# Performance work log

Measured on AMD Instinct MI355X. Metric: run time of the kernel, lower is better.

## Reference

```python
import jax, jax.numpy as jnp
import numpy as np

N = 10000
E = 160000
F_IN = 64
HID = 128
HEADS = 8
NC = 3
NEG_SLOPE = 0.2
EPS = 1e-16


def setup_inputs() -> dict:
    key = jax.random.key(0)
    ks = jax.random.split(key, 12)
    p = lambda k, shape: jax.random.normal(k, shape, jnp.float32) * 0.1
    return {
        "x": jax.random.normal(ks[0], (N, F_IN), jnp.float32),
        "edge_index": jax.random.randint(ks[1], (2, E), 0, N),
        # conv1: F_IN -> 8 heads x 128, concat -> 1024
        "W1": p(ks[2], (F_IN, HEADS * HID)),
        "a_src1": p(ks[3], (HEADS, HID)),
        "a_dst1": p(ks[4], (HEADS, HID)),
        "b1": jnp.zeros((HEADS * HID,), jnp.float32),
        # conv2: 1024 -> 8 heads x 64, concat -> 512
        "W2": p(ks[5], (HEADS * HID, HEADS * (HID // 2))),
        "a_src2": p(ks[6], (HEADS, HID // 2)),
        "a_dst2": p(ks[7], (HEADS, HID // 2)),
        "b2": jnp.zeros((HEADS * (HID // 2),), jnp.float32),
        # conv3: 512 -> 1 head x 3, mean (concat=False)
        "W3": p(ks[8], (HEADS * (HID // 2), NC)),
        "a_src3": p(ks[9], (1, NC)),
        "a_dst3": p(ks[10], (1, NC)),
        "b3": jnp.zeros((NC,), jnp.float32),
    }


def gat_conv(x, src, dst, W, a_src, a_dst, b, concat):
    """PyG-style GATConv (eval mode, self-loops already in src/dst)."""
    n = x.shape[0]
    H, C = a_src.shape
    h = (x @ W).reshape(n, H, C)                      # [N, H, C]
    s_src = jnp.sum(h * a_src[None], axis=-1)         # [N, H]
    s_dst = jnp.sum(h * a_dst[None], axis=-1)         # [N, H]
    e = jax.nn.leaky_relu(s_src[src] + s_dst[dst], NEG_SLOPE)  # [E, H]
    # segment softmax over incoming edges per destination node
    m = jax.ops.segment_max(e, dst, num_segments=n)   # [N, H]
    ex = jnp.exp(e - m[dst])
    denom = jax.ops.segment_sum(ex, dst, num_segments=n)
    alpha = ex / (denom[dst] + EPS)                   # [E, H]
    msg = h[src] * alpha[:, :, None]                  # [E, H, C]
    out = jax.ops.segment_sum(msg, dst, num_segments=n)  # [N, H, C]
    out = out.reshape(n, H * C) if concat else out.mean(axis=1)
    return out + b


def reference(x, edge_index, W1, a_src1, a_dst1, b1, W2, a_src2, a_dst2, b2, W3, a_src3, a_dst3, b3):
    n = x.shape[0]
    loop = jnp.arange(n, dtype=edge_index.dtype)
    src = jnp.concatenate([edge_index[0], loop])
    dst = jnp.concatenate([edge_index[1], loop])
    h = gat_conv(x, src, dst, W1, a_src1, a_dst1, b1, True)
    h = jax.nn.elu(h)
    h = gat_conv(h, src, dst, W2, a_src2, a_dst2, b2, True)
    h = jax.nn.elu(h)
    h = gat_conv(h, src, dst, W3, a_src3, a_dst3, b3, False)
    return jax.nn.log_softmax(h, axis=1)
```

## Files before the change

### kernel.cpp

```cpp
#include <hip/hip_runtime.h>
#include <math.h>

#define NEG_SLOPE 0.2f
#define EPS_DEN 1e-16f

typedef __attribute__((ext_vector_type(8))) short bf16x8;
typedef __attribute__((ext_vector_type(4))) float f32x4;

__device__ inline void split2(float a, short& hi, short& lo) {
    unsigned u = __float_as_uint(a);
    unsigned uh = (u + 0x8000u) & 0xFFFF0000u;
    float fh = __uint_as_float(uh);
    hi = (short)(uh >> 16);
    float r = a - fh;
    lo = (short)((__float_as_uint(r) + 0x8000u) >> 16);
}

__device__ inline unsigned short f2bf(float f) {
    unsigned u = __float_as_uint(f);
    return (unsigned short)((u + 0x7FFFu + ((u >> 16) & 1u)) >> 16);
}
__device__ inline float bflo(unsigned u) { return __uint_as_float(u << 16); }
__device__ inline float bfhi(unsigned u) { return __uint_as_float(u & 0xFFFF0000u); }

__global__ __launch_bounds__(256) void k_pre(const int* __restrict__ ei, int E, int Nn,
                                             int* __restrict__ counts,
                                             const float* __restrict__ x, short* __restrict__ A1, int Mp,
                                             const float* __restrict__ W1, short* __restrict__ B1t,
                                             const float* __restrict__ W2, short* __restrict__ B2t) {
    __shared__ float s[32][33];
    int t = threadIdx.x;
    int b = blockIdx.x;
    int ET = E + Nn;
    int etb = (ET + 255) / 256;
    int xb = (Mp * 64 + 255) / 256;
    if (b < etb) {
        int e = b * 256 + t;
        if (e < ET) {
            int d = (e < E) ? ei[E + e] : (e - E);
            atomicAdd(&counts[d], 1);
        }
        return;
    }
    b -= etb;
    if (b < xb) {
        int i = b * 256 + t;
        if (i < Mp * 64) {
            int row = i >> 6, c = i & 63;
            float v = (row < Nn) ? x[(size_t)row * 64 + c] : 0.f;
            short hi, lo;
            split2(v, hi, lo);
            A1[(size_t)row * 128 + c] = hi;
            A1[(size_t)row * 128 + 64 + c] = lo;
        }
        return;
    }
    b -= xb;
    const float* W; short* Bt; int K, N, dup, kb, nb;
    if (b < 64) {
        W = W1; Bt = B1t; K = 64; N = 1024; dup = 1;
        kb = b & 1; nb = b >> 1;
    } else {
        b -= 64;
        W = W2; Bt = B2t; K = 1024; N = 512; dup = 0;
        kb = b & 31; nb = b >> 5;
    }
    int k0 = kb * 32, n0 = nb * 32;
    int tx = t & 31, ty = t >> 5;
    for (int r = ty; r < 32; r += 8) s[r][tx] = W[(size_t)(k0 + r) * N + n0 + tx];
    __syncthreads();
    int ldbt = (1 + dup) * K;
    for (int r = ty; r < 32; r += 8) {
        float v = s[tx][r];
        unsigned u = __float_as_uint(v);
        short hi = (short)((u + 0x7FFFu + ((u >> 16) & 1u)) >> 16);
        size_t base = (size_t)(n0 + r) * ldbt + k0 + tx;
        Bt[base] = hi;
        if (dup) Bt[base + K] = hi;
    }
}

__global__ void k_scan(const int* __restrict__ counts, int Nn, int ET, int* __restrict__ row_off) {
    __shared__ int lds[256];
    int t = threadIdx.x;
    int chunk = (Nn + 255) / 256;
    int b0 = t * chunk, b1 = min(Nn, b0 + chunk);
    int s = 0;
    for (int i = b0; i < b1; i++) s += counts[i];
    lds[t] = s;
    __syncthreads();
    #pragma unroll
    for (int d = 1; d < 256; d <<= 1) {
        int v = (t >= d) ? lds[t - d] : 0;
        __syncthreads();
        lds[t] += v;
        __syncthreads();
    }
    int run = (t == 0) ? 0 : lds[t - 1];
    for (int i = b0; i < b1; i++) { row_off[i] = run; run += counts[i]; }
    if (t == 0) row_off[Nn] = ET;
}

__global__ void k_scatter(const int* __restrict__ ei, int E, int Nn,
                          const int* __restrict__ row_off, int* cursor, int* __restrict__ col) {
    int e = blockIdx.x * blockDim.x + threadIdx.x;
    int ET = E + Nn;
    if (e >= ET) return;
    int d = (e < E) ? ei[E + e] : (e - E);
    int s = (e < E) ? ei[e] : (e - E);
    int pos = atomicAdd(&cursor[d], 1);
    col[row_off[d] + pos] = s;
}

__global__ __launch_bounds__(256) void k_mfma_w(const short* __restrict__ A,
                                                const short* __restrict__ B,
                                                unsigned short* __restrict__ C,
                                                const float* __restrict__ a_src,
                                                const float* __restrict__ a_dst,
                                                float* __restrict__ ssrc,
                                                float* __restrict__ sdst,
                                                int M, int N, int Ktot,
                                                int lda, int ldb) {
    __shared__ short As[64 * 32];
    __shared__ short Bs[128 * 32];
    __shared__ float sred[4][64][2];
    int t = threadIdx.x;
    int lane = t & 63;
    int wid = t >> 6;

    int nbx = N >> 7;
    int nb = gridDim.x;
    int q = nb >> 3, r = nb & 7;
    int xcd = blockIdx.x & 7, pos = blockIdx.x >> 3;
    int L = (xcd < r ? xcd * (q + 1) : r * (q + 1) + (xcd - r) * q) + pos;
    int bn = (L % nbx) * 128;
    int bm = (L / nbx) * 64;

    int wm = (wid & 1) * 32, wn = (wid >> 1) * 64;
    int fr = lane & 15, kq = lane >> 4;

    int srow = t >> 2, sslot = t & 3;
    int sko = ((sslot ^ ((srow >> 1) & 3)) << 3);

    f32x4 acc[2][4] = {};

    for (int k0 = 0; k0 < Ktot; k0 += 32) {
        {
            const short* sa = A + (size_t)(bm + srow) * lda + k0 + sko;
            short* da = As + (size_t)(wid << 6) * 8;
            __builtin_amdgcn_global_load_lds((const __attribute__((address_space(1))) void*)sa,
                                             (__attribute__((address_space(3))) void*)da, 16, 0, 0);
            #pragma unroll
            for (int qq = 0; qq < 2; qq++) {
                int v = qq * 256 + t;
                int rowb = v >> 2, slotb = v & 3;
                int skob = ((slotb ^ ((rowb >> 1) & 3)) << 3);
                const short* sb = B + (size_t)(bn + rowb) * ldb + k0 + skob;
                short* db = Bs + (size_t)(qq * 256 + (wid << 6)) * 8;
                __builtin_amdgcn_global_load_lds((const __attribute__((address_space(1))) void*)sb,
                                                 (__attribute__((address_space(3))) void*)db, 16, 0, 0);
            }
        }
        __syncthreads();
        bf16x8 af[2], bfv[4];
        #pragma unroll
        for (int i = 0; i < 2; i++) {
            int rowa = wm + i * 16 + fr;
            af[i] = *(const bf16x8*)(As + rowa * 32 + ((kq ^ ((rowa >> 1) & 3)) << 3));
        }
        #pragma unroll
        for (int j = 0; j < 4; j++) {
            int rowb = wn + j * 16 + fr;
            bfv[j] = *(const bf16x8*)(Bs + rowb * 32 + ((kq ^ ((rowb >> 1) & 3)) << 3));
        }
        #pragma unroll
        for (int i = 0; i < 2; i++)
            #pragma unroll
            for (int j = 0; j < 4; j++)
                acc[i][j] = __builtin_amdgcn_mfma_f32_16x16x32_bf16(af[i], bfv[j], acc[i][j], 0, 0, 0);
        __syncthreads();
    }
    #pragma unroll
    for (int i = 0; i < 2; i++) {
        int rbase = bm + wm + i * 16 + kq * 4;
        #pragma unroll
        for (int j = 0; j < 4; j++) {
            int colc = bn + wn + j * 16 + fr;
            #pragma unroll
            for (int rg = 0; rg < 4; rg++) {
                int rr = rbase + rg;
                if (rr < M) C[(size_t)rr * N + colc] = f2bf(acc[i][j][rg]);
            }
        }
    }
    float asv[4], adv[4];
    #pragma unroll
    for (int j = 0; j < 4; j++) {
        int colc = bn + wn + j * 16 + fr;
        asv[j] = a_src[colc];
        adv[j] = a_dst[colc];
    }
    float ps[8], pd[8];
    #pragma unroll
    for (int i = 0; i < 2; i++)
        #pragma unroll
        for (int rg = 0; rg < 4; rg++) {
            int k8 = i * 4 + rg;
            ps[k8] = acc[i][0][rg] * asv[0] + acc[i][1][rg] * asv[1]
                   + acc[i][2][rg] * asv[2] + acc[i][3][rg] * asv[3];
            pd[k8] = acc[i][0][rg] * adv[0] + acc[i][1][rg] * adv[1]
                   + acc[i][2][rg] * adv[2] + acc[i][3][rg] * adv[3];
        }
    #pragma unroll
    for (int k8 = 0; k8 < 8; k8++) {
        #pragma unroll
        for (int off = 1; off < 16; off <<= 1) {
            ps[k8] += __shfl_xor(ps[k8], off);
            pd[k8] += __shfl_xor(pd[k8], off);
        }
    }
    if (fr == 0) {
        #pragma unroll
        for (int i = 0; i < 2; i++)
            #pragma unroll
            for (int rg = 0; rg < 4; rg++) {
                int rl = wm + i * 16 + kq * 4 + rg;
                sred[wid][rl][0] = ps[i * 4 + rg];
                sred[wid][rl][1] = pd[i * 4 + rg];
            }
    }
    __syncthreads();
    if (wid < 2 && fr == 0) {
        int hh = bn >> 7;
        #pragma unroll
        for (int i = 0; i < 2; i++)
            #pragma unroll
            for (int rg = 0; rg < 4; rg++) {
                int rl = wm + i * 16 + kq * 4 + rg;
                int rr = bm + rl;
                if (rr < M) {
                    ssrc[rr * 8 + hh] = sred[wid][rl][0] + sred[wid + 2][rl][0];
                    sdst[rr * 8 + hh] = sred[wid][rl][1] + sred[wid + 2][rl][1];
                }
            }
    }
}

__global__ __launch_bounds__(256) void k_mfma64(const short* __restrict__ A,
                                                const short* __restrict__ B,
                                                unsigned short* __restrict__ C,
                                                const float* __restrict__ a_src,
                                                const float* __restrict__ a_dst,
                                                float* __restrict__ ssrc,
                                                float* __restrict__ sdst,
                                                int M, int N, int Ktot,
                                                int lda, int ldb) {
    __shared__ short As[64 * 32];
    __shared__ short Bs[64 * 32];
    __shared__ float sred[4][64][2];
    int t = threadIdx.x;
    int lane = t & 63;
    int wid = t >> 6;

    int nbx = N >> 6;
    int nb = gridDim.x;
    int q = nb >> 3, r = nb & 7;
    int xcd = blockIdx.x & 7, pos = blockIdx.x >> 3;
    int L = (xcd < r ? xcd * (q + 1) : r * (q + 1) + (xcd - r) * q) + pos;
    int bn = (L % nbx) * 64;
    int bm = (L / nbx) * 64;

    int wm = (wid >> 1) * 32, wn = (wid & 1) * 32;
    int fr = lane & 15, kq = lane >> 4;

    int srow = t >> 2, sslot = t & 3;
    int sko = ((sslot ^ ((srow >> 1) & 3)) << 3);

    f32x4 acc[2][2] = {};

    for (int k0 = 0; k0 < Ktot; k0 += 32) {
        {
            const short* sa = A + (size_t)(bm + srow) * lda + k0 + sko;
            const short* sb = B + (size_t)(bn + srow) * ldb + k0 + sko;
            short* da = As + (size_t)(wid << 6) * 8;
            short* db = Bs + (size_t)(wid << 6) * 8;
            __builtin_amdgcn_global_load_lds((const __attribute__((address_space(1))) void*)sa,
                                             (__attribute__((address_space(3))) void*)da, 16, 0, 0);
            __builtin_amdgcn_global_load_lds((const __attribute__((address_space(1))) void*)sb,
                                             (__attribute__((address_space(3))) void*)db, 16, 0, 0);
        }
        __syncthreads();
        bf16x8 af[2], bfv[2];
        #pragma unroll
        for (int i = 0; i < 2; i++) {
            int rowa = wm + i * 16 + fr;
            int rowb = wn + i * 16 + fr;
            af[i]  = *(const bf16x8*)(As + rowa * 32 + ((kq ^ ((rowa >> 1) & 3)) << 3));
            bfv[i] = *(const bf16x8*)(Bs + rowb * 32 + ((kq ^ ((rowb >> 1) & 3)) << 3));
        }
        #pragma unroll
        for (int i = 0; i < 2; i++)
            #pragma unroll
            for (int j = 0; j < 2; j++)
                acc[i][j] = __builtin_amdgcn_mfma_f32_16x16x32_bf16(af[i], bfv[j], acc[i][j], 0, 0, 0);
        __syncthreads();
    }
    #pragma unroll
    for (int i = 0; i < 2; i++) {
        int rbase = bm + wm + i * 16 + kq * 4;
        #pragma unroll
        for (int j = 0; j < 2; j++) {
            int colc = bn + wn + j * 16 + fr;
            #pragma unroll
            for (int rg = 0; rg < 4; rg++) {
                int rr = rbase + rg;
                if (rr < M) C[(size_t)rr * N + colc] = f2bf(acc[i][j][rg]);
            }
        }
    }
    float asv[2], adv[2];
    #pragma unroll
    for (int j = 0; j < 2; j++) {
        int colc = bn + wn + j * 16 + fr;
        asv[j] = a_src[colc];
        adv[j] = a_dst[colc];
    }
    float ps[8], pd[8];
    #pragma unroll
    for (int i = 0; i < 2; i++)
        #pragma unroll
        for (int rg = 0; rg < 4; rg++) {
            int k8 = i * 4 + rg;
            ps[k8] = acc[i][0][rg] * asv[0] + acc[i][1][rg] * asv[1];
            pd[k8] = acc[i][0][rg] * adv[0] + acc[i][1][rg] * adv[1];
        }
    #pragma unroll
    for (int k8 = 0; k8 < 8; k8++) {
        #pragma unroll
        for (int off = 1; off < 16; off <<= 1) {
            ps[k8] += __shfl_xor(ps[k8], off);
            pd[k8] += __shfl_xor(pd[k8], off);
        }
    }
    if (fr == 0) {
        #pragma unroll
        for (int i = 0; i < 2; i++)
            #pragma unroll
            for (int rg = 0; rg < 4; rg++) {
                int rl = wm + i * 16 + kq * 4 + rg;
                sred[wid][rl][0] = ps[i * 4 + rg];
                sred[wid][rl][1] = pd[i * 4 + rg];
            }
    }
    __syncthreads();
    if ((wid & 1) == 0 && fr == 0) {
        int hh = bn >> 6;
        #pragma unroll
        for (int i = 0; i < 2; i++)
            #pragma unroll
            for (int rg = 0; rg < 4; rg++) {
                int rl = wm + i * 16 + kq * 4 + rg;
                int rr = bm + rl;
                if (rr < M) {
                    ssrc[rr * 8 + hh] = sred[wid][rl][0] + sred[wid | 1][rl][0];
                    sdst[rr * 8 + hh] = sred[wid][rl][1] + sred[wid | 1][rl][1];
                }
            }
    }
}

template<int H, int C, int CB, bool ELU, bool BFOUT>
__global__ __launch_bounds__(256) void k_agg_wave(const unsigned short* __restrict__ hsrc,
                                                  const float* __restrict__ ssrc,
                                                  const float* __restrict__ sdst,
                                                  const int* __restrict__ col,
                                                  const int* __restrict__ row_off,
                                                  const float* __restrict__ bias,
                                                  float* __restrict__ out,
                                                  unsigned short* __restrict__ osp,
                                                  int nw) {
    constexpr int D = H * C;
    int lane = threadIdx.x & 63;
    int w = blockIdx.x * 4 + (threadIdx.x >> 6);
    if (w >= nw) return;
    int n, cb;
    if (CB == 2) { n = w >> 1; cb = w & 1; } else { n = w; cb = 0; }
    int col0 = cb * 512 + lane * 8;
    int myhead = col0 / C;
    float sd = sdst[n * H + myhead];
    int beg = row_off[n], end = row_off[n + 1];
    const unsigned short* hbase = hsrc + col0;

    float acc[8] = {0.f, 0.f, 0.f, 0.f, 0.f, 0.f, 0.f, 0.f};
    float den = 0.f;
    #pragma unroll 4
    for (int j = beg; j < end; j++) {
        int cj = col[j];
        float s = ssrc[cj * H + myhead] + sd;
        s = (s >= 0.f) ? s : NEG_SLOPE * s;
        float ex = __expf(s);
        den += ex;
        uint4 u = *(const uint4*)(hbase + (size_t)cj * D);
        acc[0] += ex * bflo(u.x); acc[1] += ex * bfhi(u.x);
        acc[2] += ex * bflo(u.y); acc[3] += ex * bfhi(u.y);
        acc[4] += ex * bflo(u.z); acc[5] += ex * bfhi(u.z);
        acc[6] += ex * bflo(u.w); acc[7] += ex * bfhi(u.w);
    }
    float iv = 1.f / (den + EPS_DEN);
    float vals[8];
    #pragma unroll
    for (int v = 0; v < 8; v++) {
        float val = acc[v] * iv + bias[col0 + v];
        if (ELU) val = (val > 0.f) ? val : (__expf(val) - 1.f);
        vals[v] = val;
    }
    if (BFOUT) {
        uint4 o;
        o.x = (unsigned)f2bf(vals[0]) | ((unsigned)f2bf(vals[1]) << 16);
        o.y = (unsigned)f2bf(vals[2]) | ((unsigned)f2bf(vals[3]) << 16);
        o.z = (unsigned)f2bf(vals[4]) | ((unsigned)f2bf(vals[5]) << 16);
        o.w = (unsigned)f2bf(vals[6]) | ((unsigned)f2bf(vals[7]) << 16);
        *(uint4*)(osp + (size_t)n * D + col0) = o;
    } else {
        *(f32x4*)(out + (size_t)n * D + col0) = *(f32x4*)&vals[0];
        *(f32x4*)(out + (size_t)n * D + col0 + 4) = *(f32x4*)&vals[4];
    }
}

__global__ __launch_bounds__(256) void k_agg2_l3(const unsigned short* __restrict__ hsrc,
                                                 const float* __restrict__ ssrc,
                                                 const float* __restrict__ sdst,
                                                 const int* __restrict__ col,
                                                 const int* __restrict__ row_off,
                                                 const float* __restrict__ bias,
                                                 const float* __restrict__ W3,
                                                 const float* __restrict__ as3,
                                                 const float* __restrict__ ad3,
                                                 float* __restrict__ h3,
                                                 float* __restrict__ ssrc3,
                                                 float* __restrict__ sdst3,
                                                 int Nn) {
    constexpr int D = 512;
    int lane = threadIdx.x & 63;
    int n = blockIdx.x * 4 + (threadIdx.x >> 6);
    if (n >= Nn) return;
    int col0 = lane * 8;
    int myhead = lane >> 3;
    float sd = sdst[n * 8 + myhead];
    int beg = row_off[n], end = row_off[n + 1];
    const unsigned short* hbase = hsrc + col0;

    float acc[8] = {0.f, 0.f, 0.f, 0.f, 0.f, 0.f, 0.f, 0.f};
    float den = 0.f;
    #pragma unroll 4
    for (int j = beg; j < end; j++) {
        int cj = col[j];
        float s = ssrc[cj * 8 + myhead] + sd;
        s = (s >= 0.f) ? s : NEG_SLOPE * s;
        float ex = __expf(s);
        den += ex;
        uint4 u = *(const uint4*)(hbase + (size_t)cj * D);
        acc[0] += ex * bflo(u.x); acc[1] += ex * bfhi(u.x);
        acc[2] += ex * bflo(u.y); acc[3] += ex * bfhi(u.y);
        acc[4] += ex * bflo(u.z); acc[5] += ex * bfhi(u.z);
        acc[6] += ex * bflo(u.w); acc[7] += ex * bfhi(u.w);
    }
    float iv = 1.f / (den + EPS_DEN);
    float t0 = 0.f, t1 = 0.f, t2 = 0.f;
    #pragma unroll
    for (int v = 0; v < 8; v++) {
        float val = acc[v] * iv + bias[col0 + v];
        val = (val > 0.f) ? val : (__expf(val) - 1.f);
        const float* wp = W3 + (size_t)(col0 + v) * 3;
        t0 += val * wp[0];
        t1 += val * wp[1];
        t2 += val * wp[2];
    }
    #pragma unroll
    for (int off = 32; off >= 1; off >>= 1) {
        t0 += __shfl_xor(t0, off);
        t1 += __shfl_xor(t1, off);
        t2 += __shfl_xor(t2, off);
    }
    if (lane == 0) {
        h3[n * 3 + 0] = t0; h3[n * 3 + 1] = t1; h3[n * 3 + 2] = t2;
        ssrc3[n] = t0 * as3[0] + t1 * as3[1] + t2 * as3[2];
        sdst3[n] = t0 * ad3[0] + t1 * ad3[1] + t2 * ad3[2];
    }
}

__global__ __launch_bounds__(256) void k_l3_fused(const float* __restrict__ h3, const float* __restrict__ ssrc,
                                                  const float* __restrict__ sdst, const int* __restrict__ col,
                                                  const int* __restrict__ row_off, const float* __restrict__ b3,
                                                  float* __restrict__ out, int Nn) {
    int n = blockIdx.x * 64 + (threadIdx.x >> 2);
    int l4 = threadIdx.x & 3;
    if (n >= Nn) return;
    int beg = row_off[n], end = row_off[n + 1];
    float sd = sdst[n];
    float den = 0.f, a0 = 0.f, a1 = 0.f, a2 = 0.f;
    for (int j = beg + l4; j < end; j += 4) {
        int sI = col[j];
        float s = ssrc[sI] + sd;
        s = (s >= 0.f) ? s : NEG_SLOPE * s;
        float ex = __expf(s);
        den += ex;
        a0 += ex * h3[sI * 3 + 0];
        a1 += ex * h3[sI * 3 + 1];
        a2 += ex * h3[sI * 3 + 2];
    }
    #pragma unroll
    for (int off = 1; off <= 2; off <<= 1) {
        den += __shfl_xor(den, off);
        a0 += __shfl_xor(a0, off);
        a1 += __shfl_xor(a1, off);
        a2 += __shfl_xor(a2, off);
    }
    if (l4 == 0) {
        float iv = 1.f / (den + EPS_DEN);
        float v0 = a0 * iv + b3[0], v1 = a1 * iv + b3[1], v2 = a2 * iv + b3[2];
        float m = fmaxf(v0, fmaxf(v1, v2));
        float l = logf(__expf(v0 - m) + __expf(v1 - m) + __expf(v2 - m));
        out[n * 3 + 0] = v0 - m - l;
        out[n * 3 + 1] = v1 - m - l;
        out[n * 3 + 2] = v2 - m - l;
    }
}

extern "C" void kernel_launch(void* const* d_in, const int* in_sizes, int n_in,
                              void* d_out, int out_size, void* d_ws, size_t ws_size,
                              hipStream_t stream) {
    (void)n_in; (void)out_size; (void)ws_size;
    const float* x   = (const float*)d_in[0];
    const int*   ei  = (const int*)d_in[1];
    const float* W1  = (const float*)d_in[2];
    const float* as1 = (const float*)d_in[3];
    const float* ad1 = (const float*)d_in[4];
    const float* b1  = (const float*)d_in[5];
    const float* W2  = (const float*)d_in[6];
    const float* as2 = (const float*)d_in[7];
    const float* ad2 = (const float*)d_in[8];
    const float* b2  = (const float*)d_in[9];
    const float* W3  = (const float*)d_in[10];
    const float* as3 = (const float*)d_in[11];
    const float* ad3 = (const float*)d_in[12];
    const float* b3  = (const float*)d_in[13];
    float* out = (float*)d_out;

    const int Nn = in_sizes[0] / 64;
    const int E  = in_sizes[1] / 2;
    const int ET = E + Nn;
    const int Mp = ((Nn + 127) / 128) * 128;

    char* ws = (char*)d_ws;
    size_t off = 0;
    auto alloc = [&](size_t bytes) -> void* {
        void* p = ws + off;
        off = (off + bytes + 255) & ~(size_t)255;
        return p;
    };
    unsigned short* hbuf = (unsigned short*)alloc((size_t)Mp * 1024 * 2);
    unsigned short* A2   = (unsigned short*)alloc((size_t)Mp * 1024 * 2);
    float* h3   = (float*)alloc((size_t)Nn * 3 * 4);
    short* A1   = (short*)alloc((size_t)Mp * 128 * 2);
    short* B1t  = (short*)alloc((size_t)1024 * 128 * 2);
    short* B2t  = (short*)alloc((size_t)512 * 1024 * 2);
    float* ssrc = (float*)alloc((size_t)Nn * 8 * 4);
    float* sdst = (float*)alloc((size_t)Nn * 8 * 4);
    float* ssrcB= (float*)alloc((size_t)Nn * 8 * 4);
    float* sdstB= (float*)alloc((size_t)Nn * 8 * 4);
    float* ssrc3= (float*)alloc((size_t)Nn * 4);
    float* sdst3= (float*)alloc((size_t)Nn * 4);
    int* counts = (int*)alloc((size_t)Nn * 2 * 4);
    int* cursor = counts + Nn;
    int* row_off= (int*)alloc((size_t)(Nn + 1) * 4);
    int* colb   = (int*)alloc((size_t)ET * 4);

    hipMemsetAsync(counts, 0, (size_t)Nn * 2 * 4, stream);

    int etb = (ET + 255) / 256;
    int xb = (Mp * 64 + 255) / 256;
    int preb = etb + xb + 64 + 512;
    k_pre<<<preb, 256, 0, stream>>>(ei, E, Nn, counts, x, A1, Mp, W1, B1t, W2, B2t);
    k_scan<<<1, 256, 0, stream>>>(counts, Nn, ET, row_off);
    k_scatter<<<etb, 256, 0, stream>>>(ei, E, Nn, row_off, cursor, colb);

    {
        int nb = (1024 / 128) * (Mp / 64);
        k_mfma_w<<<nb, 256, 0, stream>>>(A1, B1t, hbuf, as1, ad1, ssrc, sdst,
                                         Nn, 1024, 128, 128, 128);
        int nw = Nn * 2;
        k_agg_wave<8, 128, 2, true, true><<<(nw + 3) / 4, 256, 0, stream>>>(
            hbuf, ssrc, sdst, colb, row_off, b1, nullptr, A2, nw);
    }
    {
        int nb = (512 / 64) * (Mp / 64);
        k_mfma64<<<nb, 256, 0, stream>>>((const short*)A2, B2t, hbuf, as2, ad2, ssrcB, sdstB,
                                         Nn, 512, 1024, 1024, 1024);
        k_agg2_l3<<<(Nn + 3) / 4, 256, 0, stream>>>(hbuf, ssrcB, sdstB, colb, row_off, b2,
                                                    W3, as3, ad3, h3, ssrc3, sdst3, Nn);
    }
    k_l3_fused<<<(Nn + 63) / 64, 256, 0, stream>>>(h3, ssrc3, sdst3, colb, row_off, b3, out, Nn);
}
```

Baseline: 171.7 us.

## Reuse wide-tile GEMM for layer 2 and split layer-2 aggregation across two waves

Layer 2's GEMM drops the dedicated 64x64 tile kernel and uses the templated 64x128 MFMA kernel. With 64-column heads, each wave pair computes its head's attention scores directly, with no LDS cross-wave reduction. The layer-2 aggregation now assigns two waves per node, each handling alternate edges, and combines partial sums through shared memory. This aims to raise memory-level parallelism in the gather, at the cost of an extra barrier and LDS traffic, and it doubles the grid size.

```diff
diff --git a/kernel.cpp b/kernel.cpp
--- a/kernel.cpp
+++ b/kernel.cpp
@@ -112,6 +112,7 @@
     col[row_off[d] + pos] = s;
 }
 
+template<int HEADC>
 __global__ __launch_bounds__(256) void k_mfma_w(const short* __restrict__ A,
                                                 const short* __restrict__ B,
                                                 unsigned short* __restrict__ C,
@@ -219,153 +220,46 @@
             pd[k8] += __shfl_xor(pd[k8], off);
         }
     }
-    if (fr == 0) {
-        #pragma unroll
-        for (int i = 0; i < 2; i++)
+    if (HEADC == 128) {
+        if (fr == 0) {
             #pragma unroll
-            for (int rg = 0; rg < 4; rg++) {
-                int rl = wm + i * 16 + kq * 4 + rg;
-                sred[wid][rl][0] = ps[i * 4 + rg];
-                sred[wid][rl][1] = pd[i * 4 + rg];
-            }
-    }
-    __syncthreads();
-    if (wid < 2 && fr == 0) {
-        int hh = bn >> 7;
-        #pragma unroll
-        for (int i = 0; i < 2; i++)
+            for (int i = 0; i < 2; i++)
+                #pragma unroll
+                for (int rg = 0; rg < 4; rg++) {
+                    int rl = wm + i * 16 + kq * 4 + rg;
+                    sred[wid][rl][0] = ps[i * 4 + rg];
+                    sred[wid][rl][1] = pd[i * 4 + rg];
+                }
+        }
+        __syncthreads();
+        if (wid < 2 && fr == 0) {
+            int hh = bn >> 7;
             #pragma unroll
-            for (int rg = 0; rg < 4; rg++) {
-                int rl = wm + i * 16 + kq * 4 + rg;
-                int rr = bm + rl;
-                if (rr < M) {
-                    ssrc[rr * 8 + hh] = sred[wid][rl][0] + sred[wid + 2][rl][0];
-                    sdst[rr * 8 + hh] = sred[wid][rl][1] + sred[wid + 2][rl][1];
+            for (int i = 0; i < 2; i++)
+                #pragma unroll
+                for (int rg = 0; rg < 4; rg++) {
+                    int rl = wm + i * 16 + kq * 4 + rg;
+                    int rr = bm + rl;
+                    if (rr < M) {
+                        ssrc[rr * 8 + hh] = sred[wid][rl][0] + sred[wid + 2][rl][0];
+                        sdst[rr * 8 + hh] = sred[wid][rl][1] + sred[wid + 2][rl][1];
+                    }
                 }
-            }
-    }
-}
-
-__global__ __launch_bounds__(256) void k_mfma64(const short* __restrict__ A,
-                                                const short* __restrict__ B,
-                                                unsigned short* __restrict__ C,
-                                                const float* __restrict__ a_src,
-                                                const float* __restrict__ a_dst,
-                                                float* __restrict__ ssrc,
-                                                float* __restrict__ sdst,
-                                                int M, int N, int Ktot,
-                                                int lda, int ldb) {
-    __shared__ short As[64 * 32];
-    __shared__ short Bs[64 * 32];
-    __shared__ float sred[4][64][2];
-    int t = threadIdx.x;
-    int lane = t & 63;
-    int wid = t >> 6;
-
-    int nbx = N >> 6;
-    int nb = gridDim.x;
-    int q = nb >> 3, r = nb & 7;
-    int xcd = blockIdx.x & 7, pos = blockIdx.x >> 3;
-    int L = (xcd < r ? xcd * (q + 1) : r * (q + 1) + (xcd - r) * q) + pos;
-    int bn = (L % nbx) * 64;
-    int bm = (L / nbx) * 64;
-
-    int wm = (wid >> 1) * 32, wn = (wid & 1) * 32;
-    int fr = lane & 15, kq = lane >> 4;
-
-    int srow = t >> 2, sslot = t & 3;
-    int sko = ((sslot ^ ((srow >> 1) & 3)) << 3);
-
-    f32x4 acc[2][2] = {};
-
-    for (int k0 = 0; k0 < Ktot; k0 += 32) {
-        {
-            const short* sa = A + (size_t)(bm + srow) * lda + k0 + sko;
-            const short* sb = B + (size_t)(bn + srow) * ldb + k0 + sko;
-            short* da = As + (size_t)(wid << 6) * 8;
-            short* db = Bs + (size_t)(wid << 6) * 8;
-            __builtin_amdgcn_global_load_lds((const __attribute__((address_space(1))) void*)sa,
-                                             (__attribute__((address_space(3))) void*)da, 16, 0, 0);
-            __builtin_amdgcn_global_load_lds((const __attribute__((address_space(1))) void*)sb,
-                                             (__attribute__((address_space(3))) void*)db, 16, 0, 0);
-        }
-        __syncthreads();
-        bf16x8 af[2], bfv[2];
-        #pragma unroll
-        for (int i = 0; i < 2; i++) {
-            int rowa = wm + i * 16 + fr;
-            int rowb = wn + i * 16 + fr;
-            af[i]  = *(const bf16x8*)(As + rowa * 32 + ((kq ^ ((rowa >> 1) & 3)) << 3));
-            bfv[i] = *(const bf16x8*)(Bs + rowb * 32 + ((kq ^ ((rowb >> 1) & 3)) << 3));
-        }
-        #pragma unroll
-        for (int i = 0; i < 2; i++)
+        }
+    } else {
+        int hh = (bn + wn) >> 6;
+        if (fr == 0) {
             #pragma unroll
-            for (int j = 0; j < 2; j++)
-                acc[i][j] = __builtin_amdgcn_mfma_f32_16x16x32_bf16(af[i], bfv[j], acc[i][j], 0, 0, 0);
-        __syncthreads();
-    }
-    #pragma unroll
-    for (int i = 0; i < 2; i++) {
-        int rbase = bm + wm + i * 16 + kq * 4;
-        #pragma unroll
-        for (int j = 0; j < 2; j++) {
-            int colc = bn + wn + j * 16 + fr;
-            #pragma unroll
-            for (int rg = 0; rg < 4; rg++) {
-                int rr = rbase + rg;
-                if (rr < M) C[(size_t)rr * N + colc] = f2bf(acc[i][j][rg]);
-            }
-        }
-    }
-    float asv[2], adv[2];
-    #pragma unroll
-    for (int j = 0; j < 2; j++) {
-        int colc = bn + wn + j * 16 + fr;
-        asv[j] = a_src[colc];
-        adv[j] = a_dst[colc];
-    }
-    float ps[8], pd[8];
-    #pragma unroll
-    for (int i = 0; i < 2; i++)
-        #pragma unroll
-        for (int rg = 0; rg < 4; rg++) {
-            int k8 = i * 4 + rg;
-            ps[k8] = acc[i][0][rg] * asv[0] + acc[i][1][rg] * asv[1];
-            pd[k8] = acc[i][0][rg] * adv[0] + acc[i][1][rg] * adv[1];
-        }
-    #pragma unroll
-    for (int k8 = 0; k8 < 8; k8++) {
-        #pragma unroll
-        for (int off = 1; off < 16; off <<= 1) {
-            ps[k8] += __shfl_xor(ps[k8], off);
-            pd[k8] += __shfl_xor(pd[k8], off);
-        }
-    }
-    if (fr == 0) {
-        #pragma unroll
-        for (int i = 0; i < 2; i++)
-            #pragma unroll
-            for (int rg = 0; rg < 4; rg++) {
-                int rl = wm + i * 16 + kq * 4 + rg;
-                sred[wid][rl][0] = ps[i * 4 + rg];
-                sred[wid][rl][1] = pd[i * 4 + rg];
-            }
-    }
-    __syncthreads();
-    if ((wid & 1) == 0 && fr == 0) {
-        int hh = bn >> 6;
-        #pragma unroll
-        for (int i = 0; i < 2; i++)
-            #pragma unroll
-            for (int rg = 0; rg < 4; rg++) {
-                int rl = wm + i * 16 + kq * 4 + rg;
-                int rr = bm + rl;
-                if (rr < M) {
-                    ssrc[rr * 8 + hh] = sred[wid][rl][0] + sred[wid | 1][rl][0];
-                    sdst[rr * 8 + hh] = sred[wid][rl][1] + sred[wid | 1][rl][1];
+            for (int i = 0; i < 2; i++)
+                #pragma unroll
+                for (int rg = 0; rg < 4; rg++) {
+                    int rr = bm + wm + i * 16 + kq * 4 + rg;
+                    if (rr < M) {
+                        ssrc[rr * 8 + hh] = ps[i * 4 + rg];
+                        sdst[rr * 8 + hh] = pd[i * 4 + rg];
+                    }
                 }
-            }
+        }
     }
 }
 
@@ -441,51 +335,67 @@
                                                  float* __restrict__ sdst3,
                                                  int Nn) {
     constexpr int D = 512;
-    int lane = threadIdx.x & 63;
-    int n = blockIdx.x * 4 + (threadIdx.x >> 6);
-    if (n >= Nn) return;
+    __shared__ float cacc[2][64][9];
+    int t = threadIdx.x;
+    int lane = t & 63;
+    int wid = t >> 6;
+    int node_i = wid >> 1, half = wid & 1;
+    int n = blockIdx.x * 2 + node_i;
+    bool active = (n < Nn);
     int col0 = lane * 8;
     int myhead = lane >> 3;
-    float sd = sdst[n * 8 + myhead];
-    int beg = row_off[n], end = row_off[n + 1];
-    const unsigned short* hbase = hsrc + col0;
-
     float acc[8] = {0.f, 0.f, 0.f, 0.f, 0.f, 0.f, 0.f, 0.f};
     float den = 0.f;
-    #pragma unroll 4
-    for (int j = beg; j < end; j++) {
-        int cj = col[j];
-        float s = ssrc[cj * 8 + myhead] + sd;
-        s = (s >= 0.f) ? s : NEG_SLOPE * s;
-        float ex = __expf(s);
-        den += ex;
-        uint4 u = *(const uint4*)(hbase + (size_t)cj * D);
-        acc[0] += ex * bflo(u.x); acc[1] += ex * bfhi(u.x);
-        acc[2] += ex * bflo(u.y); acc[3] += ex * bfhi(u.y);
-        acc[4] += ex * bflo(u.z); acc[5] += ex * bfhi(u.z);
-        acc[6] += ex * bflo(u.w); acc[7] += ex * bfhi(u.w);
-    }
-    float iv = 1.f / (den + EPS_DEN);
-    float t0 = 0.f, t1 = 0.f, t2 = 0.f;
-    #pragma unroll
-    for (int v = 0; v < 8; v++) {
-        float val = acc[v] * iv + bias[col0 + v];
-        val = (val > 0.f) ? val : (__expf(val) - 1.f);
-        const float* wp = W3 + (size_t)(col0 + v) * 3;
-        t0 += val * wp[0];
-        t1 += val * wp[1];
-        t2 += val * wp[2];
-    }
-    #pragma unroll
-    for (int off = 32; off >= 1; off >>= 1) {
-        t0 += __shfl_xor(t0, off);
-        t1 += __shfl_xor(t1, off);
-        t2 += __shfl_xor(t2, off);
-    }
-    if (lane == 0) {
-        h3[n * 3 + 0] = t0; h3[n * 3 + 1] = t1; h3[n * 3 + 2] = t2;
-        ssrc3[n] = t0 * as3[0] + t1 * as3[1] + t2 * as3[2];
-        sdst3[n] = t0 * ad3[0] + t1 * ad3[1] + t2 * ad3[2];
+    if (active) {
+        float sd = sdst[n * 8 + myhead];
+        int beg = row_off[n], end = row_off[n + 1];
+        const unsigned short* hbase = hsrc + col0;
+        #pragma unroll 4
+        for (int j = beg + half; j < end; j += 2) {
+            int cj = col[j];
+            float s = ssrc[cj * 8 + myhead] + sd;
+            s = (s >= 0.f) ? s : NEG_SLOPE * s;
+            float ex = __expf(s);
+            den += ex;
+            uint4 u = *(const uint4*)(hbase + (size_t)cj * D);
+            acc[0] += ex * bflo(u.x); acc[1] += ex * bfhi(u.x);
+            acc[2] += ex * bflo(u.y); acc[3] += ex * bfhi(u.y);
+            acc[4] += ex * bflo(u.z); acc[5] += ex * bfhi(u.z);
+            acc[6] += ex * bflo(u.w); acc[7] += ex * bfhi(u.w);
+        }
+    }
+    if (half == 1) {
+        #pragma unroll
+        for (int v = 0; v < 8; v++) cacc[node_i][lane][v] = acc[v];
+        cacc[node_i][lane][8] = den;
+    }
+    __syncthreads();
+    if (half == 0 && active) {
+        #pragma unroll
+        for (int v = 0; v < 8; v++) acc[v] += cacc[node_i][lane][v];
+        den += cacc[node_i][lane][8];
+        float iv = 1.f / (den + EPS_DEN);
+        float t0 = 0.f, t1 = 0.f, t2 = 0.f;
+        #pragma unroll
+        for (int v = 0; v < 8; v++) {
+            float val = acc[v] * iv + bias[col0 + v];
+            val = (val > 0.f) ? val : (__expf(val) - 1.f);
+            const float* wp = W3 + (size_t)(col0 + v) * 3;
+            t0 += val * wp[0];
+            t1 += val * wp[1];
+            t2 += val * wp[2];
+        }
+        #pragma unroll
+        for (int off = 32; off >= 1; off >>= 1) {
+            t0 += __shfl_xor(t0, off);
+            t1 += __shfl_xor(t1, off);
+            t2 += __shfl_xor(t2, off);
+        }
+        if (lane == 0) {
+            h3[n * 3 + 0] = t0; h3[n * 3 + 1] = t1; h3[n * 3 + 2] = t2;
+            ssrc3[n] = t0 * as3[0] + t1 * as3[1] + t2 * as3[2];
+            sdst3[n] = t0 * ad3[0] + t1 * ad3[1] + t2 * ad3[2];
+        }
     }
 }
 
@@ -587,17 +497,17 @@
 
     {
         int nb = (1024 / 128) * (Mp / 64);
-        k_mfma_w<<<nb, 256, 0, stream>>>(A1, B1t, hbuf, as1, ad1, ssrc, sdst,
-                                         Nn, 1024, 128, 128, 128);
+        k_mfma_w<128><<<nb, 256, 0, stream>>>(A1, B1t, hbuf, as1, ad1, ssrc, sdst,
+                                              Nn, 1024, 128, 128, 128);
         int nw = Nn * 2;
         k_agg_wave<8, 128, 2, true, true><<<(nw + 3) / 4, 256, 0, stream>>>(
             hbuf, ssrc, sdst, colb, row_off, b1, nullptr, A2, nw);
     }
     {
-        int nb = (512 / 64) * (Mp / 64);
-        k_mfma64<<<nb, 256, 0, stream>>>((const short*)A2, B2t, hbuf, as2, ad2, ssrcB, sdstB,
-                                         Nn, 512, 1024, 1024, 1024);
-        k_agg2_l3<<<(Nn + 3) / 4, 256, 0, stream>>>(hbuf, ssrcB, sdstB, colb, row_off, b2,
+        int nb = (512 / 128) * (Mp / 64);
+        k_mfma_w<64><<<nb, 256, 0, stream>>>((const short*)A2, B2t, hbuf, as2, ad2, ssrcB, sdstB,
+                                             Nn, 512, 1024, 1024, 1024);
+        k_agg2_l3<<<(Nn + 1) / 2, 256, 0, stream>>>(hbuf, ssrcB, sdstB, colb, row_off, b2,
                                                     W3, as3, ad3, h3, ssrc3, sdst3, Nn);
     }
     k_l3_fused<<<(Nn + 63) / 64, 256, 0, stream>>>(h3, ssrc3, sdst3, colb, row_off, b3, out, Nn);
```

Result: no change. 169.3 us (-1.4%).
